# Optimization experiments

Hardware: AMD Instinct MI355X
Metric: run time of the kernel (lower is better)

## Reference

```python
import jax, jax.numpy as jnp
import numpy as np

EPS = 1e-05
N_HEADS = 16
HEAD_DIM = 64

def rms_norm(x, w, eps=EPS):
    # RMSNorm over last dim, computed in float32 then cast back (matches torch source)
    xf = x.astype(jnp.float32)
    out = xf * jax.lax.rsqrt(jnp.mean(xf * xf, axis=-1, keepdims=True) + eps)
    return (out * w).astype(x.dtype)

def split_heads(x, heads):
    # Faithful to reshape_heads: (B,T,C) -> (B,T,C//heads,heads) -> (B,heads,T,C//heads)
    B, T, C = x.shape
    return x.reshape(B, T, C // heads, heads).transpose(0, 3, 1, 2)

def setup_inputs() -> dict:
    key = jax.random.key(0)
    ks = jax.random.split(key, 5)
    B, T, D = 2, 2048, 1024
    s = 0.02
    return {
        "x": jax.random.normal(ks[0], (B, T, D), dtype=jnp.float32),
        "wq": jax.random.normal(ks[1], (D, N_HEADS * HEAD_DIM), dtype=jnp.float32) * s,
        "wk": jax.random.normal(ks[2], (D, N_HEADS * HEAD_DIM), dtype=jnp.float32) * s,
        "wv": jax.random.normal(ks[3], (D, N_HEADS * HEAD_DIM), dtype=jnp.float32) * s,
        "wo": jax.random.normal(ks[4], (N_HEADS * HEAD_DIM, D), dtype=jnp.float32) * s,
        "q_norm_w": jnp.ones((HEAD_DIM,), dtype=jnp.float32),
        "k_norm_w": jnp.ones((HEAD_DIM,), dtype=jnp.float32),
    }

def reference(x, wq, wk, wv, wo, q_norm_w, k_norm_w):
    B, T, D = x.shape
    # QKV projections (no bias)
    q = split_heads(x @ wq, N_HEADS)   # [B,H,T,hd]
    k = split_heads(x @ wk, N_HEADS)
    v = split_heads(x @ wv, N_HEADS)
    # per-head qk RMSNorm
    q = rms_norm(q, q_norm_w)
    k = rms_norm(k, k_norm_w)
    # scaled dot-product attention
    scale = 1.0 / jnp.sqrt(jnp.array(HEAD_DIM, dtype=x.dtype))
    scores = jnp.einsum('bhqd,bhkd->bhqk', q, k) * scale  # [B,H,T,T]
    attn = jax.nn.softmax(scores, axis=-1)
    out = jnp.einsum('bhqk,bhkd->bhqd', attn, v)           # [B,H,T,hd]
    # rearrange 'b h n d -> b n (h d)'
    out = out.transpose(0, 2, 1, 3).reshape(B, T, N_HEADS * HEAD_DIM)
    return out @ wo
```

## Files before the change

### kernel.cpp

```cpp
#include <hip/hip_runtime.h>

typedef _Float16 f16;
typedef _Float16 f16x8 __attribute__((ext_vector_type(8)));
typedef _Float16 f16x4 __attribute__((ext_vector_type(4)));
typedef float    f32x4 __attribute__((ext_vector_type(4)));

#define DEV __device__ __forceinline__

static constexpr int Tn = 2048;
static constexpr int Dn = 1024;
static constexpr int Mn = 2 * Tn;
static constexpr int NQKV = 3 * Dn;

DEV void gld16(const void* g, void* l) {
  __builtin_amdgcn_global_load_lds((const __attribute__((address_space(1))) unsigned int*)g,
                                   (__attribute__((address_space(3))) unsigned int*)l, 16, 0, 0);
}

DEV void st_pk(void* p, float a, float b) {
  auto v = __builtin_amdgcn_cvt_pkrtz(a, b);
  *(unsigned int*)p = __builtin_bit_cast(unsigned int, v);
}

__global__ __launch_bounds__(256) void k_prep(const float* __restrict__ x, const float* __restrict__ wq,
                                              const float* __restrict__ wk, const float* __restrict__ wv,
                                              const float* __restrict__ wo, f16* __restrict__ xb,
                                              f16* __restrict__ wcat_t, f16* __restrict__ wot) {
  int bid = blockIdx.x;
  if (bid < 4096) {
    int i = bid * 256 + threadIdx.x;
    float4 v = ((const float4*)x)[i];
    f16x4 o4; o4.x = (f16)v.x; o4.y = (f16)v.y; o4.z = (f16)v.z; o4.w = (f16)v.w;
    ((f16x4*)xb)[i] = o4;
    return;
  }
  __shared__ float tile[64][65];
  int wb = bid - 4096;
  int z = wb >> 8;
  int rb = wb & 255;
  int k0 = (rb >> 4) * 64, n0 = (rb & 15) * 64;
  const float* srcs[4] = {wq, wk, wv, wo};
  const float* w = srcs[z];
  f16* dst = (z == 3) ? wot : wcat_t + (size_t)z * Dn * Dn;
#pragma unroll
  for (int p = 0; p < 16; ++p) {
    int flat = threadIdx.x + p * 256;
    int kl = flat >> 6, nl = flat & 63;
    tile[kl][nl] = w[(size_t)(k0 + kl) * Dn + n0 + nl];
  }
  __syncthreads();
#pragma unroll
  for (int p = 0; p < 16; ++p) {
    int flat = threadIdx.x + p * 256;
    int nl = flat >> 6, kl = flat & 63;
    int c = n0 + nl;
    int cp = (z == 3) ? c : (((c & 15) << 6) | (c >> 4));
    dst[(size_t)cp * Dn + k0 + kl] = (f16)tile[kl][nl];
  }
}

__global__ __launch_bounds__(256) void k_gemm_qkv(const f16* __restrict__ A, const f16* __restrict__ Bt,
                                                  const float* __restrict__ qw, const float* __restrict__ kw,
                                                  f16* __restrict__ qatt, f16* __restrict__ katt,
                                                  f16* __restrict__ vatt) {
  constexpr int K = 1024;
  __shared__ __align__(16) f16 As[128 * 64];
  __shared__ __align__(16) f16 Bs[128 * 64];
  const int lane = threadIdx.x & 63, wid = threadIdx.x >> 6;
  const int m0 = blockIdx.y * 128;
  const int n0 = blockIdx.x * 128;
  const int wr = (wid >> 1) * 64, wc = (wid & 1) * 64;
  f32x4 acc[4][4];
#pragma unroll
  for (int i = 0; i < 4; ++i)
#pragma unroll
    for (int j = 0; j < 4; ++j) acc[i][j] = (f32x4){0.f, 0.f, 0.f, 0.f};

  char* AsB = (char*)As; char* BsB = (char*)Bs;
  for (int k0 = 0; k0 < K; k0 += 64) {
    __syncthreads();
#pragma unroll
    for (int it = 0; it < 4; ++it) {
      int flat = ((wid * 4 + it) * 64 + lane) * 16;
      int row = flat >> 7, g = (flat >> 4) & 7;
      int sw = (g ^ (row & 7)) << 4;
      gld16((const char*)A + ((size_t)(m0 + row) * K + k0) * 2 + sw, AsB + (wid * 4 + it) * 1024);
      gld16((const char*)Bt + ((size_t)(n0 + row) * K + k0) * 2 + sw, BsB + (wid * 4 + it) * 1024);
    }
    __syncthreads();
#pragma unroll
    for (int kk = 0; kk < 2; ++kk) {
      f16x8 af[4], bf[4];
#pragma unroll
      for (int ms = 0; ms < 4; ++ms) {
        int r = wr + ms * 16 + (lane & 15);
        af[ms] = *(const f16x8*)(AsB + r * 128 + (((kk * 4 + (lane >> 4)) ^ (r & 7)) << 4));
      }
#pragma unroll
      for (int ns = 0; ns < 4; ++ns) {
        int r = wc + ns * 16 + (lane & 15);
        bf[ns] = *(const f16x8*)(BsB + r * 128 + (((kk * 4 + (lane >> 4)) ^ (r & 7)) << 4));
      }
#pragma unroll
      for (int ms = 0; ms < 4; ++ms)
#pragma unroll
        for (int ns = 0; ns < 4; ++ns)
          acc[ms][ns] = __builtin_amdgcn_mfma_f32_16x16x32_f16(af[ms], bf[ns], acc[ms][ns], 0, 0, 0);
    }
  }

  const int rq = lane >> 4, cq = lane & 15;
  const int sec = blockIdx.x >> 3;
  const int hwave = (((blockIdx.x & 7) * 128) + wc) >> 6;
  f16* dst = (sec == 0) ? qatt : (sec == 1) ? katt : vatt;
  float wv[4];
#pragma unroll
  for (int ns = 0; ns < 4; ++ns) {
    if (sec == 0)      wv[ns] = qw[ns * 16 + cq] * 0.18033688011116013f;
    else if (sec == 1) wv[ns] = kw[ns * 16 + cq];
    else               wv[ns] = 1.f;
  }
#pragma unroll
  for (int ms = 0; ms < 4; ++ms) {
#pragma unroll
    for (int r = 0; r < 4; ++r) {
      int row = m0 + wr + ms * 16 + rq * 4 + r;
      float sc = 1.f;
      if (sec < 2) {
        float ss = 0.f;
#pragma unroll
        for (int ns = 0; ns < 4; ++ns) ss += acc[ms][ns][r] * acc[ms][ns][r];
        ss += __shfl_xor(ss, 1, 64);
        ss += __shfl_xor(ss, 2, 64);
        ss += __shfl_xor(ss, 4, 64);
        ss += __shfl_xor(ss, 8, 64);
        sc = rsqrtf(ss * (1.f / 64) + 1e-5f);
      }
      int b = row >> 11, t = row & 2047;
      size_t base = ((size_t)(b * 16 + hwave) * Tn + t) * 64;
#pragma unroll
      for (int ns = 0; ns < 4; ++ns)
        dst[base + ns * 16 + cq] = (f16)(acc[ms][ns][r] * sc * wv[ns]);
    }
  }
}

__global__ __launch_bounds__(256) void k_vtrans(const f16* __restrict__ vatt, f16* __restrict__ vt) {
  __shared__ f16 tile[64][72];
  int t0 = blockIdx.x * 64, bh = blockIdx.y;
  const f16* src = vatt + ((size_t)bh * Tn + t0) * 64;
#pragma unroll
  for (int p = 0; p < 2; ++p) {
    int c = threadIdx.x + p * 256;
    int tl = c >> 3, dc = (c & 7) * 8;
    f16x8 v = *(const f16x8*)(src + (size_t)tl * 64 + dc);
#pragma unroll
    for (int j = 0; j < 8; ++j) tile[dc + j][tl] = v[j];
  }
  __syncthreads();
#pragma unroll
  for (int p = 0; p < 2; ++p) {
    int c = threadIdx.x + p * 256;
    int d = c >> 3, tc = (c & 7) * 8;
    f16x8 o;
#pragma unroll
    for (int j = 0; j < 8; ++j) o[j] = tile[d][tc + j];
    *(f16x8*)(vt + ((size_t)bh * 64 + d) * Tn + t0 + tc) = o;
  }
}

__global__ __launch_bounds__(256) void k_attn(const f16* __restrict__ qatt, const f16* __restrict__ katt,
                                              const f16* __restrict__ vt, f16* __restrict__ attout) {
  __shared__ __align__(16) f16 Ks[2][64 * 64];
  __shared__ __align__(16) f16 Vs[2][64 * 64];
  __shared__ __align__(16) f16 Ps[4][1024];
  const int lane = threadIdx.x & 63, wid = threadIdx.x >> 6;
  const int q = lane & 15, g = lane >> 4;
  const int bh = blockIdx.y, b = bh >> 4, h = bh & 15;
  const int tq0 = blockIdx.x * 64 + wid * 16;

  const f16* qbase = qatt + ((size_t)bh * Tn + tq0) * 64;
  f16x8 qf[2];
#pragma unroll
  for (int kk = 0; kk < 2; ++kk)
    qf[kk] = *(const f16x8*)(qbase + (size_t)q * 64 + kk * 32 + g * 8);

  f32x4 o[4];
#pragma unroll
  for (int i = 0; i < 4; ++i) o[i] = (f32x4){0.f, 0.f, 0.f, 0.f};
  float psum = 0.f;

  const char* kgb = (const char*)(katt + (size_t)bh * Tn * 64);
  const char* vgb = (const char*)(vt + (size_t)bh * 64 * Tn);
  char* KsB = (char*)Ks; char* VsB = (char*)Vs;
  char* PsB = (char*)Ps + wid * 2048;
  const int xq = (q & 7) << 4;
  char* pwr[4];
#pragma unroll
  for (int sub = 0; sub < 4; ++sub)
    pwr[sub] = PsB + q * 128 + ((g & 1) * 8) + ((((sub * 2) + (g >> 1)) ^ (q & 7)) << 4);
  const char* prd0 = PsB + q * 128 + ((g * 16) ^ xq);
  const char* prd1 = PsB + q * 128 + (((64 + g * 16)) ^ xq);

  auto stage = [&](int buf, int kt) {
    int k0 = kt * 64;
#pragma unroll
    for (int it = 0; it < 2; ++it) {
      int flat = ((wid * 2 + it) * 64 + lane) * 16;
      int row = flat >> 7, gg = (flat >> 4) & 7;
      int sw = (gg ^ (row & 7)) << 4;
      gld16(kgb + ((size_t)(k0 + row) * 64) * 2 + sw, KsB + buf * 8192 + (wid * 2 + it) * 1024);
      gld16(vgb + ((size_t)row * Tn + k0) * 2 + sw, VsB + buf * 8192 + (wid * 2 + it) * 1024);
    }
  };

  constexpr int NT = Tn / 64;
  stage(0, 0);

  for (int kt = 0; kt < NT; ++kt) {
    const int cur = kt & 1;
    const char* Kc = KsB + cur * 8192;
    const char* Vc = VsB + cur * 8192;
    if (kt + 1 < NT) {
      stage(cur ^ 1, kt + 1);
      asm volatile("s_waitcnt vmcnt(4)" ::: "memory");
    } else {
      asm volatile("s_waitcnt vmcnt(0)" ::: "memory");
    }
    __builtin_amdgcn_s_barrier();
    __builtin_amdgcn_sched_barrier(0);

    f32x4 s[4];
    __builtin_amdgcn_s_setprio(1);
#pragma unroll
    for (int sub = 0; sub < 4; ++sub) {
      s[sub] = (f32x4){0.f, 0.f, 0.f, 0.f};
#pragma unroll
      for (int kk = 0; kk < 2; ++kk) {
        int kr = sub * 16 + q;
        f16x8 kf = *(const f16x8*)(Kc + kr * 128 + (((kk * 4 + g) ^ (kr & 7)) << 4));
        s[sub] = __builtin_amdgcn_mfma_f32_16x16x32_f16(kf, qf[kk], s[sub], 0, 0, 0);
      }
    }
    __builtin_amdgcn_s_setprio(0);

#pragma unroll
    for (int sub = 0; sub < 2; ++sub) {
      float e0 = __builtin_amdgcn_exp2f(s[sub][0]);
      float e1 = __builtin_amdgcn_exp2f(s[sub][1]);
      float e2 = __builtin_amdgcn_exp2f(s[sub][2]);
      float e3 = __builtin_amdgcn_exp2f(s[sub][3]);
      psum += (e0 + e1) + (e2 + e3);
      st_pk(pwr[sub],     e0, e1);
      st_pk(pwr[sub] + 4, e2, e3);
    }
    f16x8 pa0 = *(const f16x8*)prd0;
#pragma unroll
    for (int sub = 2; sub < 4; ++sub) {
      float e0 = __builtin_amdgcn_exp2f(s[sub][0]);
      float e1 = __builtin_amdgcn_exp2f(s[sub][1]);
      float e2 = __builtin_amdgcn_exp2f(s[sub][2]);
      float e3 = __builtin_amdgcn_exp2f(s[sub][3]);
      psum += (e0 + e1) + (e2 + e3);
      st_pk(pwr[sub],     e0, e1);
      st_pk(pwr[sub] + 4, e2, e3);
    }
    f16x8 pa1 = *(const f16x8*)prd1;

    __builtin_amdgcn_s_setprio(1);
#pragma unroll
    for (int ds = 0; ds < 4; ++ds) {
      int dr = ds * 16 + q;
      f16x8 vb0 = *(const f16x8*)(Vc + dr * 128 + (((0 + g) ^ (dr & 7)) << 4));
      o[ds] = __builtin_amdgcn_mfma_f32_16x16x32_f16(pa0, vb0, o[ds], 0, 0, 0);
      f16x8 vb1 = *(const f16x8*)(Vc + dr * 128 + (((4 + g) ^ (dr & 7)) << 4));
      o[ds] = __builtin_amdgcn_mfma_f32_16x16x32_f16(pa1, vb1, o[ds], 0, 0, 0);
    }
    __builtin_amdgcn_s_setprio(0);
    __builtin_amdgcn_s_barrier();
  }

  psum += __shfl_xor(psum, 16, 64);
  psum += __shfl_xor(psum, 32, 64);
  float invq = 1.f / psum;
  float inv[4];
#pragma unroll
  for (int r = 0; r < 4; ++r)
    inv[r] = __int_as_float(__builtin_amdgcn_ds_bpermute(((g * 4 + r)) << 2, __float_as_int(invq)));
#pragma unroll
  for (int ds = 0; ds < 4; ++ds)
#pragma unroll
    for (int r = 0; r < 4; ++r) {
      int t = tq0 + g * 4 + r;
      attout[((size_t)(b * Tn + t)) * Dn + h * 64 + ds * 16 + q] = (f16)(o[ds][r] * inv[r]);
    }
}

__global__ __launch_bounds__(256) void k_gemm_o(const f16* __restrict__ A, const f16* __restrict__ Bt,
                                                float* __restrict__ C, int N, int K) {
  __shared__ __align__(16) f16 As[64 * 64];
  __shared__ __align__(16) f16 Bs[128 * 64];
  const int lane = threadIdx.x & 63, wid = threadIdx.x >> 6;
  const int m0 = blockIdx.y * 64, n0 = blockIdx.x * 128;
  const int wr = (wid >> 1) * 32, wc = (wid & 1) * 64;
  f32x4 acc[2][4];
#pragma unroll
  for (int i = 0; i < 2; ++i)
#pragma unroll
    for (int j = 0; j < 4; ++j) acc[i][j] = (f32x4){0.f, 0.f, 0.f, 0.f};

  char* AsB = (char*)As; char* BsB = (char*)Bs;
  for (int k0 = 0; k0 < K; k0 += 64) {
    __syncthreads();
#pragma unroll
    for (int it = 0; it < 2; ++it) {
      int flat = ((wid * 2 + it) * 64 + lane) * 16;
      int row = flat >> 7, g = (flat >> 4) & 7;
      int sw = (g ^ (row & 7)) << 4;
      gld16((const char*)A + ((size_t)(m0 + row) * K + k0) * 2 + sw, AsB + (wid * 2 + it) * 1024);
    }
#pragma unroll
    for (int it = 0; it < 4; ++it) {
      int flat = ((wid * 4 + it) * 64 + lane) * 16;
      int row = flat >> 7, g = (flat >> 4) & 7;
      int sw = (g ^ (row & 7)) << 4;
      gld16((const char*)Bt + ((size_t)(n0 + row) * K + k0) * 2 + sw, BsB + (wid * 4 + it) * 1024);
    }
    __syncthreads();
#pragma unroll
    for (int kk = 0; kk < 2; ++kk) {
      f16x8 af[2], bf[4];
#pragma unroll
      for (int ms = 0; ms < 2; ++ms) {
        int r = wr + ms * 16 + (lane & 15);
        af[ms] = *(const f16x8*)(AsB + r * 128 + (((kk * 4 + (lane >> 4)) ^ (r & 7)) << 4));
      }
#pragma unroll
      for (int ns = 0; ns < 4; ++ns) {
        int r = wc + ns * 16 + (lane & 15);
        bf[ns] = *(const f16x8*)(BsB + r * 128 + (((kk * 4 + (lane >> 4)) ^ (r & 7)) << 4));
      }
#pragma unroll
      for (int ms = 0; ms < 2; ++ms)
#pragma unroll
        for (int ns = 0; ns < 4; ++ns)
          acc[ms][ns] = __builtin_amdgcn_mfma_f32_16x16x32_f16(af[ms], bf[ns], acc[ms][ns], 0, 0, 0);
    }
  }
  const int rq = lane >> 4, cq = lane & 15;
#pragma unroll
  for (int ms = 0; ms < 2; ++ms)
#pragma unroll
    for (int ns = 0; ns < 4; ++ns)
#pragma unroll
      for (int r = 0; r < 4; ++r)
        C[(size_t)(m0 + wr + ms * 16 + rq * 4 + r) * N + n0 + wc + ns * 16 + cq] = acc[ms][ns][r];
}

extern "C" void kernel_launch(void* const* d_in, const int* in_sizes, int n_in,
                              void* d_out, int out_size, void* d_ws, size_t ws_size,
                              hipStream_t stream) {
  const float* x  = (const float*)d_in[0];
  const float* wq = (const float*)d_in[1];
  const float* wk = (const float*)d_in[2];
  const float* wv = (const float*)d_in[3];
  const float* wo = (const float*)d_in[4];
  const float* qw = (const float*)d_in[5];
  const float* kw = (const float*)d_in[6];

  char* ws = (char*)d_ws;
  const size_t MB = 1 << 20;
  f16* xb     = (f16*)(ws + 0 * MB);
  f16* wcat   = (f16*)(ws + 8 * MB);
  f16* wot    = (f16*)(ws + 14 * MB);
  f16* qatt   = (f16*)(ws + 16 * MB);
  f16* katt   = (f16*)(ws + 24 * MB);
  f16* vatt   = (f16*)(ws + 32 * MB);
  f16* vtb    = (f16*)(ws + 40 * MB);
  f16* attout = (f16*)(ws + 48 * MB);

  k_prep<<<dim3(5120), 256, 0, stream>>>(x, wq, wk, wv, wo, xb, wcat, wot);
  k_gemm_qkv<<<dim3(NQKV / 128, Mn / 128), 256, 0, stream>>>(xb, wcat, qw, kw, qatt, katt, vatt);
  k_vtrans<<<dim3(Tn / 64, 32), 256, 0, stream>>>(vatt, vtb);
  k_attn<<<dim3(Tn / 64, 32), 256, 0, stream>>>(qatt, katt, vtb, attout);
  k_gemm_o<<<dim3(Dn / 128, Mn / 64), 256, 0, stream>>>(attout, wot, (float*)d_out, Dn, Dn);
}
```

Before: 215.1 us.

## Double query rows per wave, keep P in registers, stage output through LDS

Each wave in the attention kernel now handles 32 query rows instead of 16, so every K and V fragment read from LDS feeds twice as many MFMAs. The P matrix no longer round-trips through shared memory: it is packed into registers and used directly as the B operand of 16x16x16 MFMAs, which removes the Ps buffer and its stores and loads. The output tile is written into the freed K buffer and then stored to global memory with coalesced 16-byte writes. In exchange the kernel uses more registers, which may lower occupancy, and launches half as many blocks.

```diff
diff --git a/kernel.cpp b/kernel.cpp
--- a/kernel.cpp
+++ b/kernel.cpp
@@ -17,9 +17,11 @@
                                    (__attribute__((address_space(3))) unsigned int*)l, 16, 0, 0);
 }
 
-DEV void st_pk(void* p, float a, float b) {
-  auto v = __builtin_amdgcn_cvt_pkrtz(a, b);
-  *(unsigned int*)p = __builtin_bit_cast(unsigned int, v);
+DEV f16x4 pk4(float a, float b, float c, float d) {
+  unsigned int lo = __builtin_bit_cast(unsigned int, __builtin_amdgcn_cvt_pkrtz(a, b));
+  unsigned int hi = __builtin_bit_cast(unsigned int, __builtin_amdgcn_cvt_pkrtz(c, d));
+  unsigned long long u = (unsigned long long)lo | ((unsigned long long)hi << 32);
+  return __builtin_bit_cast(f16x4, u);
 }
 
 __global__ __launch_bounds__(256) void k_prep(const float* __restrict__ x, const float* __restrict__ wq,
@@ -173,34 +175,29 @@
                                               const f16* __restrict__ vt, f16* __restrict__ attout) {
   __shared__ __align__(16) f16 Ks[2][64 * 64];
   __shared__ __align__(16) f16 Vs[2][64 * 64];
-  __shared__ __align__(16) f16 Ps[4][1024];
   const int lane = threadIdx.x & 63, wid = threadIdx.x >> 6;
   const int q = lane & 15, g = lane >> 4;
   const int bh = blockIdx.y, b = bh >> 4, h = bh & 15;
-  const int tq0 = blockIdx.x * 64 + wid * 16;
+  const int tq0 = blockIdx.x * 128 + wid * 32;
 
   const f16* qbase = qatt + ((size_t)bh * Tn + tq0) * 64;
-  f16x8 qf[2];
-#pragma unroll
-  for (int kk = 0; kk < 2; ++kk)
-    qf[kk] = *(const f16x8*)(qbase + (size_t)q * 64 + kk * 32 + g * 8);
-
-  f32x4 o[4];
-#pragma unroll
-  for (int i = 0; i < 4; ++i) o[i] = (f32x4){0.f, 0.f, 0.f, 0.f};
-  float psum = 0.f;
+  f16x8 qf[2][2];
+#pragma unroll
+  for (int qg = 0; qg < 2; ++qg)
+#pragma unroll
+    for (int kk = 0; kk < 2; ++kk)
+      qf[qg][kk] = *(const f16x8*)(qbase + (size_t)(qg * 16 + q) * 64 + kk * 32 + g * 8);
+
+  f32x4 o[4][2];
+#pragma unroll
+  for (int i = 0; i < 4; ++i)
+#pragma unroll
+    for (int j = 0; j < 2; ++j) o[i][j] = (f32x4){0.f, 0.f, 0.f, 0.f};
+  float psum[2] = {0.f, 0.f};
 
   const char* kgb = (const char*)(katt + (size_t)bh * Tn * 64);
   const char* vgb = (const char*)(vt + (size_t)bh * 64 * Tn);
   char* KsB = (char*)Ks; char* VsB = (char*)Vs;
-  char* PsB = (char*)Ps + wid * 2048;
-  const int xq = (q & 7) << 4;
-  char* pwr[4];
-#pragma unroll
-  for (int sub = 0; sub < 4; ++sub)
-    pwr[sub] = PsB + q * 128 + ((g & 1) * 8) + ((((sub * 2) + (g >> 1)) ^ (q & 7)) << 4);
-  const char* prd0 = PsB + q * 128 + ((g * 16) ^ xq);
-  const char* prd1 = PsB + q * 128 + (((64 + g * 16)) ^ xq);
 
   auto stage = [&](int buf, int kt) {
     int k0 = kt * 64;
@@ -230,70 +227,80 @@
     __builtin_amdgcn_s_barrier();
     __builtin_amdgcn_sched_barrier(0);
 
-    f32x4 s[4];
+    f32x4 s[4][2];
     __builtin_amdgcn_s_setprio(1);
 #pragma unroll
     for (int sub = 0; sub < 4; ++sub) {
-      s[sub] = (f32x4){0.f, 0.f, 0.f, 0.f};
-#pragma unroll
-      for (int kk = 0; kk < 2; ++kk) {
-        int kr = sub * 16 + q;
-        f16x8 kf = *(const f16x8*)(Kc + kr * 128 + (((kk * 4 + g) ^ (kr & 7)) << 4));
-        s[sub] = __builtin_amdgcn_mfma_f32_16x16x32_f16(kf, qf[kk], s[sub], 0, 0, 0);
+      int kr = sub * 16 + q;
+      f16x8 kf0 = *(const f16x8*)(Kc + kr * 128 + (((0 + g) ^ (kr & 7)) << 4));
+      f16x8 kf1 = *(const f16x8*)(Kc + kr * 128 + (((4 + g) ^ (kr & 7)) << 4));
+#pragma unroll
+      for (int qg = 0; qg < 2; ++qg) {
+        f32x4 z = (f32x4){0.f, 0.f, 0.f, 0.f};
+        z = __builtin_amdgcn_mfma_f32_16x16x32_f16(kf0, qf[qg][0], z, 0, 0, 0);
+        s[sub][qg] = __builtin_amdgcn_mfma_f32_16x16x32_f16(kf1, qf[qg][1], z, 0, 0, 0);
       }
     }
     __builtin_amdgcn_s_setprio(0);
 
-#pragma unroll
-    for (int sub = 0; sub < 2; ++sub) {
-      float e0 = __builtin_amdgcn_exp2f(s[sub][0]);
-      float e1 = __builtin_amdgcn_exp2f(s[sub][1]);
-      float e2 = __builtin_amdgcn_exp2f(s[sub][2]);
-      float e3 = __builtin_amdgcn_exp2f(s[sub][3]);
-      psum += (e0 + e1) + (e2 + e3);
-      st_pk(pwr[sub],     e0, e1);
-      st_pk(pwr[sub] + 4, e2, e3);
-    }
-    f16x8 pa0 = *(const f16x8*)prd0;
-#pragma unroll
-    for (int sub = 2; sub < 4; ++sub) {
-      float e0 = __builtin_amdgcn_exp2f(s[sub][0]);
-      float e1 = __builtin_amdgcn_exp2f(s[sub][1]);
-      float e2 = __builtin_amdgcn_exp2f(s[sub][2]);
-      float e3 = __builtin_amdgcn_exp2f(s[sub][3]);
-      psum += (e0 + e1) + (e2 + e3);
-      st_pk(pwr[sub],     e0, e1);
-      st_pk(pwr[sub] + 4, e2, e3);
-    }
-    f16x8 pa1 = *(const f16x8*)prd1;
+    f16x4 pb[4][2];
+#pragma unroll
+    for (int sub = 0; sub < 4; ++sub)
+#pragma unroll
+      for (int qg = 0; qg < 2; ++qg) {
+        float e0 = __builtin_amdgcn_exp2f(s[sub][qg][0]);
+        float e1 = __builtin_amdgcn_exp2f(s[sub][qg][1]);
+        float e2 = __builtin_amdgcn_exp2f(s[sub][qg][2]);
+        float e3 = __builtin_amdgcn_exp2f(s[sub][qg][3]);
+        psum[qg] += (e0 + e1) + (e2 + e3);
+        pb[sub][qg] = pk4(e0, e1, e2, e3);
+      }
 
     __builtin_amdgcn_s_setprio(1);
 #pragma unroll
-    for (int ds = 0; ds < 4; ++ds) {
-      int dr = ds * 16 + q;
-      f16x8 vb0 = *(const f16x8*)(Vc + dr * 128 + (((0 + g) ^ (dr & 7)) << 4));
-      o[ds] = __builtin_amdgcn_mfma_f32_16x16x32_f16(pa0, vb0, o[ds], 0, 0, 0);
-      f16x8 vb1 = *(const f16x8*)(Vc + dr * 128 + (((4 + g) ^ (dr & 7)) << 4));
-      o[ds] = __builtin_amdgcn_mfma_f32_16x16x32_f16(pa1, vb1, o[ds], 0, 0, 0);
+    for (int dt = 0; dt < 4; ++dt) {
+      int dr = dt * 16 + q;
+#pragma unroll
+      for (int ks = 0; ks < 4; ++ks) {
+        f16x4 va = *(const f16x4*)(Vc + dr * 128 + (((ks * 2 + (g >> 1)) ^ (q & 7)) << 4) + (g & 1) * 8);
+#pragma unroll
+        for (int qg = 0; qg < 2; ++qg)
+          o[dt][qg] = __builtin_amdgcn_mfma_f32_16x16x16f16(va, pb[ks][qg], o[dt][qg], 0, 0, 0);
+      }
     }
     __builtin_amdgcn_s_setprio(0);
     __builtin_amdgcn_s_barrier();
   }
 
-  psum += __shfl_xor(psum, 16, 64);
-  psum += __shfl_xor(psum, 32, 64);
-  float invq = 1.f / psum;
-  float inv[4];
-#pragma unroll
-  for (int r = 0; r < 4; ++r)
-    inv[r] = __int_as_float(__builtin_amdgcn_ds_bpermute(((g * 4 + r)) << 2, __float_as_int(invq)));
-#pragma unroll
-  for (int ds = 0; ds < 4; ++ds)
-#pragma unroll
-    for (int r = 0; r < 4; ++r) {
-      int t = tq0 + g * 4 + r;
-      attout[((size_t)(b * Tn + t)) * Dn + h * 64 + ds * 16 + q] = (f16)(o[ds][r] * inv[r]);
-    }
+#pragma unroll
+  for (int qg = 0; qg < 2; ++qg) {
+    psum[qg] += __shfl_xor(psum[qg], 16, 64);
+    psum[qg] += __shfl_xor(psum[qg], 32, 64);
+  }
+  float inv[2] = {1.f / psum[0], 1.f / psum[1]};
+  char* TsB = (char*)Ks;
+#pragma unroll
+  for (int dt = 0; dt < 4; ++dt)
+#pragma unroll
+    for (int qg = 0; qg < 2; ++qg) {
+      f16x4 pv = pk4(o[dt][qg][0] * inv[qg], o[dt][qg][1] * inv[qg],
+                     o[dt][qg][2] * inv[qg], o[dt][qg][3] * inv[qg]);
+      int qrow = wid * 32 + qg * 16 + q;
+      int c = dt * 2 + (g >> 1);
+      char* p = TsB + qrow * 128 + ((c ^ (qrow & 7)) << 4) + (g & 1) * 8;
+      *(unsigned long long*)p = __builtin_bit_cast(unsigned long long, pv);
+    }
+  __syncthreads();
+  {
+    int qrow = threadIdx.x >> 1, half = threadIdx.x & 1;
+    f16* gdst = attout + ((size_t)(b * Tn) + blockIdx.x * 128 + qrow) * Dn + h * 64 + half * 32;
+#pragma unroll
+    for (int j = 0; j < 4; ++j) {
+      int hc = half * 4 + j;
+      f16x8 vv = *(const f16x8*)(TsB + qrow * 128 + ((hc ^ (qrow & 7)) << 4));
+      *(f16x8*)(gdst + j * 8) = vv;
+    }
+  }
 }
 
 __global__ __launch_bounds__(256) void k_gemm_o(const f16* __restrict__ A, const f16* __restrict__ Bt,
@@ -382,6 +389,6 @@
   k_prep<<<dim3(5120), 256, 0, stream>>>(x, wq, wk, wv, wo, xb, wcat, wot);
   k_gemm_qkv<<<dim3(NQKV / 128, Mn / 128), 256, 0, stream>>>(xb, wcat, qw, kw, qatt, katt, vatt);
   k_vtrans<<<dim3(Tn / 64, 32), 256, 0, stream>>>(vatt, vtb);
-  k_attn<<<dim3(Tn / 64, 32), 256, 0, stream>>>(qatt, katt, vtb, attout);
+  k_attn<<<dim3(Tn / 128, 32), 256, 0, stream>>>(qatt, katt, vtb, attout);
   k_gemm_o<<<dim3(Dn / 128, Mn / 64), 256, 0, stream>>>(attout, wot, (float*)d_out, Dn, Dn);
 }
```

New measurement: 219.1 us. About the same (+1.9%).
